# Kernel optimization log

Measured on AMD Instinct MI355X. Metric: run time of the kernel, lower is better.

Reference implementation:

```python
import jax, jax.numpy as jnp
import numpy as np

MIN_CONN, MAX_CONN = 1, 16
RATIO = 0.25
EPS_NORM = 1e-12   # F.normalize eps
GN_EPS = 1e-5
NUM_GROUPS = 32    # largest divisor of C=128 that is <= 32


def setup_inputs() -> dict:
    key = jax.random.key(0)
    ks = jax.random.split(key, 3)
    B, C, H, W = 2, 128, 48, 48
    x = jax.random.normal(ks[0], (B, C, H, W), dtype=jnp.float32)
    gamma = jnp.ones((C,), jnp.float32)
    beta = jnp.zeros((C,), jnp.float32)
    w1 = jax.random.normal(ks[1], (2 * C, C), jnp.float32) * 0.02
    b1 = jnp.zeros((2 * C,), jnp.float32)
    w2 = jax.random.normal(ks[2], (C, 2 * C), jnp.float32) * 0.02
    b2 = jnp.zeros((C,), jnp.float32)
    return {"x": x, "gamma": gamma, "beta": beta, "w1": w1, "b1": b1, "w2": w2, "b2": b2}


def _connection_counts(x):
    B, C, H, W = x.shape
    xd = jax.image.resize(x, (B, C, H // 2, W // 2), method='bilinear', antialias=False)
    xdu = jax.image.resize(xd, (B, C, H, W), method='bilinear', antialias=False)
    df = jnp.abs(x - xdu).sum(axis=1, keepdims=True)  # [B,1,H,W]
    dmin = df.reshape(B, -1).min(axis=1).reshape(B, 1, 1, 1)
    dmax = df.reshape(B, -1).max(axis=1).reshape(B, 1, 1, 1)
    dn = (df - dmin) / (dmax - dmin + 1e-8)
    return MIN_CONN + jnp.round(dn * (MAX_CONN - MIN_CONN))  # [B,1,H,W] float


def _ipg_forward(x, gamma, beta, w1, b1, w2, b2):
    B, C, H, W = x.shape
    cc = _connection_counts(x)

    win = max(3, int(min(H, W) * RATIO))
    if win % 2 == 0:
        win += 1
    K2 = win * win
    pad = win // 2

    xp = jnp.pad(x, ((0, 0), (0, 0), (pad, pad), (pad, pad)), mode='reflect')
    # unfold -> [B, C, K2, H, W] with torch ordering (row-major over (i,j))
    patches = jnp.stack([xp[:, :, i:i + H, j:j + W]
                         for i in range(win) for j in range(win)], axis=2)
    patches = patches.reshape(B, C, K2, H * W).transpose(0, 3, 1, 2)  # [B,P,C,K2]

    x_flat = x.reshape(B, C, H * W).transpose(0, 2, 1)  # [B,P,C]
    x_norm = x_flat / jnp.maximum(jnp.linalg.norm(x_flat, axis=-1, keepdims=True), EPS_NORM)
    pnorm = jnp.maximum(jnp.sqrt((patches ** 2).sum(axis=2)), EPS_NORM)  # [B,P,K2]
    sim = jnp.einsum('bpck,bpc->bpk', patches, x_norm) / pnorm  # [B,P,K2]

    # variable-k topk as a rank mask: rank(sim descending) < k, then exp-softmax over selected
    k = jnp.minimum(cc.reshape(B, H * W), float(K2))  # [B,P]
    ranks = jnp.argsort(jnp.argsort(-sim, axis=-1), axis=-1)  # [B,P,K2]
    mask = ranks < k[..., None]
    w = jnp.exp(sim) * mask
    w = w / w.sum(axis=-1, keepdims=True)
    out = jnp.einsum('bpck,bpk->bpc', patches, w)  # [B,P,C]
    out = out.transpose(0, 2, 1).reshape(B, C, H, W)

    # GroupNorm(32, C)
    xg = x.reshape(B, NUM_GROUPS, C // NUM_GROUPS, H, W)
    mu = xg.mean(axis=(2, 3, 4), keepdims=True)
    var = xg.var(axis=(2, 3, 4), keepdims=True)
    xn = ((xg - mu) / jnp.sqrt(var + GN_EPS)).reshape(B, C, H, W)
    norm_x = xn * gamma[None, :, None, None] + beta[None, :, None, None]

    enhanced = out + norm_x
    # 1x1 conv FFN
    h = jnp.einsum('oc,bchw->bohw', w1, enhanced) + b1[None, :, None, None]
    h = jax.nn.relu(h)
    ffn = jnp.einsum('oc,bchw->bohw', w2, h) + b2[None, :, None, None]
    return enhanced + ffn


def reference(x, gamma, beta, w1, b1, w2, b2):
    return _ipg_forward(x, gamma, beta, w1, b1, w2, b2)
```

## Files before the change

### kernel.cpp

```cpp
#include <hip/hip_runtime.h>

constexpr int CH = 128;
constexpr int WW = 48;
constexpr int PP = 2304;
constexpr int NPIX = 4608;
constexpr int K2 = 169;

constexpr size_t OFF_XT  = 0;
constexpr size_t OFF_RN  = OFF_XT + (size_t)NPIX * CH;
constexpr size_t OFF_DF  = OFF_RN + NPIX;
constexpr size_t OFF_GNP = OFF_DF + NPIX;
constexpr size_t OFF_MMP = OFF_GNP + 288 * 16;
constexpr size_t OFF_W1T = OFF_MMP + 144;
constexpr size_t OFF_W2T = OFF_W1T + 32768;
constexpr size_t WS_FLOATS = OFF_W2T + 32768;

__device__ __forceinline__ int refl(int t) {
    return t < 0 ? -t : (t > 47 ? 94 - t : t);
}

__global__ __launch_bounds__(256) void kA(const float* __restrict__ x,
                                          const float* __restrict__ w1,
                                          const float* __restrict__ w2,
                                          float* __restrict__ xt,
                                          float* __restrict__ gnp,
                                          float* __restrict__ w1t,
                                          float* __restrict__ w2t,
                                          float* __restrict__ df,
                                          float* __restrict__ rn,
                                          float* __restrict__ mmp) {
    __shared__ union { float t[32][65]; float red[4][64][2]; } sm;
    const int tid = threadIdx.x;
    const int bid = blockIdx.x;
    if (bid < 288) {
        const int tile = bid >> 2, q = bid & 3;
        const int p0 = tile * 64;
        const int b = p0 / PP, pb = p0 % PP;
        const int pl = tid & 63, cb = tid >> 6;
        const float* xb = x + (size_t)b * CH * PP + (size_t)(q * 32) * PP + pb;
#pragma unroll
        for (int r = 0; r < 8; r++) {
            int c = r * 4 + cb;
            sm.t[c][pl] = xb[(size_t)c * PP + pl];
        }
        __syncthreads();
        {
            const int c4 = tid & 7, pq = tid >> 3;
#pragma unroll
            for (int r = 0; r < 2; r++) {
                int px = r * 32 + pq;
                float4 v = make_float4(sm.t[c4 * 4][px], sm.t[c4 * 4 + 1][px],
                                       sm.t[c4 * 4 + 2][px], sm.t[c4 * 4 + 3][px]);
                ((float4*)(xt + (size_t)(p0 + px) * CH + q * 32))[c4] = v;
            }
        }
        {
            const int j = tid >> 5, part = tid & 31;
            float s = 0.f, sq = 0.f;
#pragma unroll
            for (int pi = 0; pi < 2; pi++) {
                int px = part * 2 + pi;
#pragma unroll
                for (int i = 0; i < 4; i++) {
                    float v = sm.t[j * 4 + i][px];
                    s += v; sq += v * v;
                }
            }
#pragma unroll
            for (int m = 16; m; m >>= 1) { s += __shfl_xor(s, m); sq += __shfl_xor(sq, m); }
            if (part == 0) { gnp[bid * 16 + j * 2] = s; gnp[bid * 16 + j * 2 + 1] = sq; }
        }
    } else if (bid < 360) {
        const int strip = bid - 288;
        const int p0 = strip * 64;
        const int b = p0 / PP;
        const int wv = tid >> 6, lane = tid & 63;
        const int p = (p0 % PP) + lane;
        const int h = p / WW, w = p % WW;
        float py = 0.5f * h - 0.25f; int y0 = (int)floorf(py); float fy = py - (float)y0;
        float px_ = 0.5f * w - 0.25f; int x0 = (int)floorf(px_); float fx = px_ - (float)x0;
        int y0c = max(y0, 0), y1c = min(y0 + 1, 23);
        int x0c = max(x0, 0), x1c = min(x0 + 1, 23);
        float q00 = 0.25f * (1.f - fy) * (1.f - fx), q01 = 0.25f * (1.f - fy) * fx;
        float q10 = 0.25f * fy * (1.f - fx),        q11 = 0.25f * fy * fx;
        int r0 = (2 * y0c) * WW, r1 = (2 * y0c + 1) * WW;
        int r2 = (2 * y1c) * WW, r3 = (2 * y1c + 1) * WW;
        int ca = 2 * x0c, cb2 = 2 * x1c;
        const float* xc = x + (size_t)b * CH * PP + (size_t)(wv * 32) * PP;
        float ds = 0.f, ss = 0.f;
        for (int c = 0; c < 32; c++) {
            const float* xp = xc + (size_t)c * PP;
            float xv = xp[p];
            float s00 = xp[r0 + ca] + xp[r0 + ca + 1] + xp[r1 + ca] + xp[r1 + ca + 1];
            float s01 = xp[r0 + cb2] + xp[r0 + cb2 + 1] + xp[r1 + cb2] + xp[r1 + cb2 + 1];
            float s10 = xp[r2 + ca] + xp[r2 + ca + 1] + xp[r3 + ca] + xp[r3 + ca + 1];
            float s11 = xp[r2 + cb2] + xp[r2 + cb2 + 1] + xp[r3 + cb2] + xp[r3 + cb2 + 1];
            float up = q00 * s00 + q01 * s01 + q10 * s10 + q11 * s11;
            ds += fabsf(xv - up);
            ss += xv * xv;
        }
        sm.red[wv][lane][0] = ds; sm.red[wv][lane][1] = ss;
        __syncthreads();
        if (wv == 0) {
            float dst = sm.red[0][lane][0] + sm.red[1][lane][0] +
                        sm.red[2][lane][0] + sm.red[3][lane][0];
            float sst = sm.red[0][lane][1] + sm.red[1][lane][1] +
                        sm.red[2][lane][1] + sm.red[3][lane][1];
            df[p0 + lane] = dst;
            rn[p0 + lane] = 1.f / fmaxf(sqrtf(sst), 1e-12f);
            float mn = dst, mx = dst;
#pragma unroll
            for (int m = 32; m; m >>= 1) {
                mn = fminf(mn, __shfl_xor(mn, m));
                mx = fmaxf(mx, __shfl_xor(mx, m));
            }
            if (lane == 0) { mmp[strip * 2] = mn; mmp[strip * 2 + 1] = mx; }
        }
    } else {
        int idx = (bid - 360) * 256 + tid;
        if (idx < 32768) {
            int o = idx >> 7, c = idx & 127;
            w1t[(size_t)((c >> 2) * 256 + o) * 4 + (c & 3)] = w1[idx];
        } else {
            int i2 = idx - 32768;
            int c = i2 >> 8, oo = i2 & 255;
            w2t[(size_t)((oo >> 2) * 128 + c) * 4 + (oo & 3)] = w2[i2];
        }
    }
}

__global__ __launch_bounds__(256, 4) void kB(const float* __restrict__ xt,
                                             const float* __restrict__ rn,
                                             const float* __restrict__ df,
                                             const float* __restrict__ mmp,
                                             const float* __restrict__ gnp,
                                             const float* __restrict__ gamma,
                                             const float* __restrict__ beta,
                                             const float* __restrict__ w1t,
                                             const float* __restrict__ w2t,
                                             const float* __restrict__ b1f,
                                             const float* __restrict__ b2f,
                                             float* __restrict__ out) {
    __shared__ union {
        float sims[4][176];
        struct { float elds[4][128]; float hlds[4][256]; } f;
    } sm;
    __shared__ float gnbl[32][2];
    __shared__ float mml[2];
    const int tid = threadIdx.x, wv = tid >> 6, lane = tid & 63;
    const int base = blockIdx.x * 4;
    const int b = base / PP;

    if (tid < 32) {
        const int g = tid, q = g >> 3, j = g & 7;
        float s = 0.f, sq = 0.f;
#pragma unroll 4
        for (int t2 = 0; t2 < 36; t2++) {
            int u = (b * 36 + t2) * 4 + q;
            s += gnp[u * 16 + j * 2];
            sq += gnp[u * 16 + j * 2 + 1];
        }
        float mu = s / 9216.f;
        float var = sq / 9216.f - mu * mu;
        gnbl[g][0] = mu;
        gnbl[g][1] = 1.f / sqrtf(var + 1e-5f);
    } else if (tid >= 64 && tid < 128) {
        int i = tid - 64;
        float mn = 1e30f, mx = -1e30f;
        if (i < 36) { mn = mmp[(b * 36 + i) * 2]; mx = mmp[(b * 36 + i) * 2 + 1]; }
#pragma unroll
        for (int m = 32; m; m >>= 1) {
            mn = fminf(mn, __shfl_xor(mn, m));
            mx = fmaxf(mx, __shfl_xor(mx, m));
        }
        if (i == 0) { mml[0] = mn; mml[1] = mx; }
    }
    __syncthreads();
    const float dmin = mml[0], dmax = mml[1];

    const int pix = base + wv;
    const int p = pix % PP;
    const int h = p / WW, w = p % WW;
    const int bb = b * PP;
    const int g8 = lane >> 3, cl = lane & 7;

    float4 ctr[4];
    const float4* cp = (const float4*)(xt + (size_t)pix * CH) + cl;
#pragma unroll
    for (int c = 0; c < 4; c++) ctr[c] = cp[c * 8];
    const float rnp = rn[pix];

    for (int kb = 0; kb < 176; kb += 8) {
        const int k = kb + g8;
        const int krow = k / 13, kcol = k - krow * 13;
        const int yy = refl(h + krow - 6), xx = refl(w + kcol - 6);
        const int p2 = bb + yy * WW + xx;
        const float4* rp = (const float4*)(xt + (size_t)p2 * CH) + cl;
        float dot = 0.f;
#pragma unroll
        for (int c = 0; c < 4; c++) {
            float4 v = rp[c * 8];
            dot += v.x * ctr[c].x + v.y * ctr[c].y + v.z * ctr[c].z + v.w * ctr[c].w;
        }
        dot += __shfl_xor(dot, 1);
        dot += __shfl_xor(dot, 2);
        dot += __shfl_xor(dot, 4);
        float s = dot * rnp * rn[p2];
        if (cl == 0 && k < K2) sm.sims[wv][k] = s;
    }

    float s0 = sm.sims[wv][lane];
    float s1 = (64 + lane < K2) ? sm.sims[wv][64 + lane] : -1e30f;
    float s2 = (128 + lane < K2) ? sm.sims[wv][128 + lane] : -1e30f;
    const float dn = (df[pix] - dmin) / (dmax - dmin + 1e-8f);
    const int cc = 1 + (int)rintf(dn * 15.f);

    float wsum = 0.f, ax = 0.f, ay = 0.f;
    for (int i = 0; i < cc; ++i) {
        float gm = fmaxf(fmaxf(s0, s1), s2);
#pragma unroll
        for (int sft = 1; sft <= 32; sft <<= 1) gm = fmaxf(gm, __shfl_xor(gm, sft));
        unsigned long long m0 = __ballot(s0 == gm);
        unsigned long long m1 = __ballot(s1 == gm);
        unsigned long long m2 = __ballot(s2 == gm);
        int kw = m0 ? (__ffsll(m0) - 1)
               : m1 ? (64 + __ffsll(m1) - 1)
                    : (128 + __ffsll(m2) - 1);
        bool me = (lane == (kw & 63));
        s0 = (me && kw < 64) ? -1e30f : s0;
        s1 = (me && kw >= 64 && kw < 128) ? -1e30f : s1;
        s2 = (me && kw >= 128) ? -1e30f : s2;
        float wt = expf(gm);
        wsum += wt;
        int krow = kw / 13, kcol = kw - krow * 13;
        int p2 = bb + refl(h + krow - 6) * WW + refl(w + kcol - 6);
        float2 v = ((const float2*)(xt + (size_t)p2 * CH))[lane];
        ax += wt * v.x; ay += wt * v.y;
    }
    const float invw = 1.f / wsum;

    float2 xv = ((const float2*)(xt + (size_t)pix * CH))[lane];
    const int c0 = lane * 2, grp = lane >> 1;
    const float mu = gnbl[grp][0], rstd = gnbl[grp][1];
    float e0 = ax * invw + (xv.x - mu) * rstd * gamma[c0] + beta[c0];
    float e1 = ay * invw + (xv.y - mu) * rstd * gamma[c0 + 1] + beta[c0 + 1];

    __syncthreads();
    ((float2*)sm.f.elds[wv])[lane] = make_float2(e0, e1);
    __syncthreads();

    {
        float acc4[4] = {0.f, 0.f, 0.f, 0.f};
        const float4* wp = ((const float4*)w1t) + tid;
        for (int c4 = 0; c4 < 32; c4++) {
            float4 wv4 = wp[c4 * 256];
#pragma unroll
            for (int px = 0; px < 4; px++) {
                float4 ev = *(const float4*)&sm.f.elds[px][c4 * 4];
                acc4[px] += wv4.x * ev.x + wv4.y * ev.y + wv4.z * ev.z + wv4.w * ev.w;
            }
        }
        float bv = b1f[tid];
#pragma unroll
        for (int px = 0; px < 4; px++)
            sm.f.hlds[px][tid] = fmaxf(acc4[px] + bv, 0.f);
    }
    __syncthreads();
    {
        const int c = tid & 127, hf = tid >> 7;
        const int px0 = hf * 2;
        float acc2[2] = {0.f, 0.f};
        const float4* wp2 = ((const float4*)w2t) + c;
        for (int o4 = 0; o4 < 64; o4++) {
            float4 wv4 = wp2[o4 * 128];
#pragma unroll
            for (int j = 0; j < 2; j++) {
                float4 hv = *(const float4*)&sm.f.hlds[px0 + j][o4 * 4];
                acc2[j] += wv4.x * hv.x + wv4.y * hv.y + wv4.z * hv.z + wv4.w * hv.w;
            }
        }
        float bv = b2f[c];
        float2 o2;
        o2.x = sm.f.elds[px0 + 0][c] + acc2[0] + bv;
        o2.y = sm.f.elds[px0 + 1][c] + acc2[1] + bv;
        *(float2*)(out + ((size_t)(b * CH + c)) * PP + (base % PP) + px0) = o2;
    }
}

extern "C" void kernel_launch(void* const* d_in, const int* in_sizes, int n_in,
                              void* d_out, int out_size, void* d_ws, size_t ws_size,
                              hipStream_t stream) {
    (void)in_sizes; (void)n_in; (void)out_size;
    if (ws_size < WS_FLOATS * sizeof(float)) return;

    const float* x     = (const float*)d_in[0];
    const float* gamma = (const float*)d_in[1];
    const float* beta  = (const float*)d_in[2];
    const float* w1    = (const float*)d_in[3];
    const float* b1    = (const float*)d_in[4];
    const float* w2    = (const float*)d_in[5];
    const float* b2    = (const float*)d_in[6];
    float* ws = (float*)d_ws;
    float* xt  = ws + OFF_XT;
    float* rn  = ws + OFF_RN;
    float* df  = ws + OFF_DF;
    float* gnp = ws + OFF_GNP;
    float* mmp = ws + OFF_MMP;
    float* w1t = ws + OFF_W1T;
    float* w2t = ws + OFF_W2T;
    float* out = (float*)d_out;

    hipLaunchKernelGGL(kA, dim3(616),  dim3(256), 0, stream,
                       x, w1, w2, xt, gnp, w1t, w2t, df, rn, mmp);
    hipLaunchKernelGGL(kB, dim3(1152), dim3(256), 0, stream,
                       xt, rn, df, mmp, gnp, gamma, beta, w1t, w2t, b1, b2, out);
}
```

Measured before the change: 63.89 us.

## Decouple top-k selection from gather and widen similarity per-lane work

The similarity loop now gives each lane group 4 lanes instead of 8, so it processes 16 neighbours per iteration with 8 float4 loads per lane, and it is unrolled by two. The serial top-k loop only records the selected indices and scores in shared memory. A separate, fully unrolled 16-iteration gather loop then does the exp and weighted accumulation, so its global loads can be issued together instead of one dependent load per selection step. Slots that were not selected hold score -1e30, so their exp is 0, but they still issue loads of neighbour 0. Launch bounds drop to 2 blocks per SM to allow more registers, at some cost in occupancy.

```diff
diff --git a/kernel.cpp b/kernel.cpp
--- a/kernel.cpp
+++ b/kernel.cpp
@@ -129,7 +129,7 @@
     }
 }
 
-__global__ __launch_bounds__(256, 4) void kB(const float* __restrict__ xt,
+__global__ __launch_bounds__(256, 2) void kB(const float* __restrict__ xt,
                                              const float* __restrict__ rn,
                                              const float* __restrict__ df,
                                              const float* __restrict__ mmp,
@@ -142,7 +142,7 @@
                                              const float* __restrict__ b2f,
                                              float* __restrict__ out) {
     __shared__ union {
-        float sims[4][176];
+        struct { float sims[4][176]; int kl[4][16]; float wl[4][16]; } a;
         struct { float elds[4][128]; float hlds[4][256]; } f;
     } sm;
     __shared__ float gnbl[32][2];
@@ -182,40 +182,41 @@
     const int p = pix % PP;
     const int h = p / WW, w = p % WW;
     const int bb = b * PP;
-    const int g8 = lane >> 3, cl = lane & 7;
-
-    float4 ctr[4];
-    const float4* cp = (const float4*)(xt + (size_t)pix * CH) + cl;
-#pragma unroll
-    for (int c = 0; c < 4; c++) ctr[c] = cp[c * 8];
+    const int g16 = lane >> 2, cl2 = lane & 3;
+
+    float4 ctr[8];
+    const float4* cp = (const float4*)(xt + (size_t)pix * CH);
+#pragma unroll
+    for (int c = 0; c < 8; c++) ctr[c] = cp[c * 4 + cl2];
     const float rnp = rn[pix];
 
-    for (int kb = 0; kb < 176; kb += 8) {
-        const int k = kb + g8;
+    if (lane < 16) { sm.a.kl[wv][lane] = 0; sm.a.wl[wv][lane] = -1e30f; }
+
+#pragma unroll 2
+    for (int kb = 0; kb < 176; kb += 16) {
+        const int k = kb + g16;
         const int krow = k / 13, kcol = k - krow * 13;
         const int yy = refl(h + krow - 6), xx = refl(w + kcol - 6);
         const int p2 = bb + yy * WW + xx;
-        const float4* rp = (const float4*)(xt + (size_t)p2 * CH) + cl;
+        const float4* rp = (const float4*)(xt + (size_t)p2 * CH);
         float dot = 0.f;
 #pragma unroll
-        for (int c = 0; c < 4; c++) {
-            float4 v = rp[c * 8];
+        for (int c = 0; c < 8; c++) {
+            float4 v = rp[c * 4 + cl2];
             dot += v.x * ctr[c].x + v.y * ctr[c].y + v.z * ctr[c].z + v.w * ctr[c].w;
         }
         dot += __shfl_xor(dot, 1);
         dot += __shfl_xor(dot, 2);
-        dot += __shfl_xor(dot, 4);
         float s = dot * rnp * rn[p2];
-        if (cl == 0 && k < K2) sm.sims[wv][k] = s;
-    }
-
-    float s0 = sm.sims[wv][lane];
-    float s1 = (64 + lane < K2) ? sm.sims[wv][64 + lane] : -1e30f;
-    float s2 = (128 + lane < K2) ? sm.sims[wv][128 + lane] : -1e30f;
+        if (cl2 == 0 && k < K2) sm.a.sims[wv][k] = s;
+    }
+
+    float s0 = sm.a.sims[wv][lane];
+    float s1 = sm.a.sims[wv][64 + lane];
+    float s2 = (128 + lane < K2) ? sm.a.sims[wv][128 + lane] : -1e30f;
     const float dn = (df[pix] - dmin) / (dmax - dmin + 1e-8f);
     const int cc = 1 + (int)rintf(dn * 15.f);
 
-    float wsum = 0.f, ax = 0.f, ay = 0.f;
     for (int i = 0; i < cc; ++i) {
         float gm = fmaxf(fmaxf(s0, s1), s2);
 #pragma unroll
@@ -230,12 +231,19 @@
         s0 = (me && kw < 64) ? -1e30f : s0;
         s1 = (me && kw >= 64 && kw < 128) ? -1e30f : s1;
         s2 = (me && kw >= 128) ? -1e30f : s2;
-        float wt = expf(gm);
-        wsum += wt;
-        int krow = kw / 13, kcol = kw - krow * 13;
-        int p2 = bb + refl(h + krow - 6) * WW + refl(w + kcol - 6);
+        if (lane == 0) { sm.a.kl[wv][i] = kw; sm.a.wl[wv][i] = gm; }
+    }
+
+    float wsum = 0.f, ax = 0.f, ay = 0.f;
+#pragma unroll
+    for (int i = 0; i < 16; ++i) {
+        const int kw = sm.a.kl[wv][i];
+        const float sv = sm.a.wl[wv][i];
+        const float wt = expf(sv);
+        const int krow = kw / 13, kcol = kw - krow * 13;
+        const int p2 = bb + refl(h + krow - 6) * WW + refl(w + kcol - 6);
         float2 v = ((const float2*)(xt + (size_t)p2 * CH))[lane];
-        ax += wt * v.x; ay += wt * v.y;
+        wsum += wt; ax += wt * v.x; ay += wt * v.y;
     }
     const float invw = 1.f / wsum;
 
```

Result: slower. 70.07 us (+9.7%).

## Split similarity computation across two wave halves and decouple top-k gather

Applied to the files above, without the earlier changes.

Doubles the kB block to 512 threads so two waves share each pixel's 169 similarity dot products, halving the serial neighbour loop per wave. The top-k selection now only records the chosen indices and scores in shared memory, and a separate fully unrolled 16-iteration loop gathers and accumulates, so the neighbour loads are independent instead of interleaved with the serial selection. Unused slots carry -1e30 so their exp contributes zero. In exchange, the extra waves sit idle during selection and the FFN stages, and each block always issues 16 gather loads.

```diff
diff --git a/kernel.cpp b/kernel.cpp
--- a/kernel.cpp
+++ b/kernel.cpp
@@ -129,7 +129,7 @@
     }
 }
 
-__global__ __launch_bounds__(256, 4) void kB(const float* __restrict__ xt,
+__global__ __launch_bounds__(512, 8) void kB(const float* __restrict__ xt,
                                              const float* __restrict__ rn,
                                              const float* __restrict__ df,
                                              const float* __restrict__ mmp,
@@ -142,12 +142,13 @@
                                              const float* __restrict__ b2f,
                                              float* __restrict__ out) {
     __shared__ union {
-        float sims[4][176];
+        struct { float sims[4][176]; int kl[4][16]; float wl[4][16]; } a;
         struct { float elds[4][128]; float hlds[4][256]; } f;
     } sm;
     __shared__ float gnbl[32][2];
     __shared__ float mml[2];
     const int tid = threadIdx.x, wv = tid >> 6, lane = tid & 63;
+    const int pxw = wv & 3, half = wv >> 2;
     const int base = blockIdx.x * 4;
     const int b = base / PP;
 
@@ -175,10 +176,8 @@
         }
         if (i == 0) { mml[0] = mn; mml[1] = mx; }
     }
-    __syncthreads();
-    const float dmin = mml[0], dmax = mml[1];
-
-    const int pix = base + wv;
+
+    const int pix = base + pxw;
     const int p = pix % PP;
     const int h = p / WW, w = p % WW;
     const int bb = b * PP;
@@ -189,9 +188,12 @@
 #pragma unroll
     for (int c = 0; c < 4; c++) ctr[c] = cp[c * 8];
     const float rnp = rn[pix];
-
-    for (int kb = 0; kb < 176; kb += 8) {
-        const int k = kb + g8;
+    __syncthreads();
+
+    const int kb0 = half * 88;
+#pragma unroll 2
+    for (int it = 0; it < 11; ++it) {
+        const int k = kb0 + it * 8 + g8;
         const int krow = k / 13, kcol = k - krow * 13;
         const int yy = refl(h + krow - 6), xx = refl(w + kcol - 6);
         const int p2 = bb + yy * WW + xx;
@@ -206,50 +208,62 @@
         dot += __shfl_xor(dot, 2);
         dot += __shfl_xor(dot, 4);
         float s = dot * rnp * rn[p2];
-        if (cl == 0 && k < K2) sm.sims[wv][k] = s;
-    }
-
-    float s0 = sm.sims[wv][lane];
-    float s1 = (64 + lane < K2) ? sm.sims[wv][64 + lane] : -1e30f;
-    float s2 = (128 + lane < K2) ? sm.sims[wv][128 + lane] : -1e30f;
-    const float dn = (df[pix] - dmin) / (dmax - dmin + 1e-8f);
-    const int cc = 1 + (int)rintf(dn * 15.f);
-
-    float wsum = 0.f, ax = 0.f, ay = 0.f;
-    for (int i = 0; i < cc; ++i) {
-        float gm = fmaxf(fmaxf(s0, s1), s2);
-#pragma unroll
-        for (int sft = 1; sft <= 32; sft <<= 1) gm = fmaxf(gm, __shfl_xor(gm, sft));
-        unsigned long long m0 = __ballot(s0 == gm);
-        unsigned long long m1 = __ballot(s1 == gm);
-        unsigned long long m2 = __ballot(s2 == gm);
-        int kw = m0 ? (__ffsll(m0) - 1)
-               : m1 ? (64 + __ffsll(m1) - 1)
-                    : (128 + __ffsll(m2) - 1);
-        bool me = (lane == (kw & 63));
-        s0 = (me && kw < 64) ? -1e30f : s0;
-        s1 = (me && kw >= 64 && kw < 128) ? -1e30f : s1;
-        s2 = (me && kw >= 128) ? -1e30f : s2;
-        float wt = expf(gm);
-        wsum += wt;
-        int krow = kw / 13, kcol = kw - krow * 13;
-        int p2 = bb + refl(h + krow - 6) * WW + refl(w + kcol - 6);
-        float2 v = ((const float2*)(xt + (size_t)p2 * CH))[lane];
-        ax += wt * v.x; ay += wt * v.y;
-    }
-    const float invw = 1.f / wsum;
-
-    float2 xv = ((const float2*)(xt + (size_t)pix * CH))[lane];
-    const int c0 = lane * 2, grp = lane >> 1;
-    const float mu = gnbl[grp][0], rstd = gnbl[grp][1];
-    float e0 = ax * invw + (xv.x - mu) * rstd * gamma[c0] + beta[c0];
-    float e1 = ay * invw + (xv.y - mu) * rstd * gamma[c0 + 1] + beta[c0 + 1];
-
-    __syncthreads();
-    ((float2*)sm.f.elds[wv])[lane] = make_float2(e0, e1);
-    __syncthreads();
-
-    {
+        if (cl == 0 && k < K2) sm.a.sims[pxw][k] = s;
+    }
+    __syncthreads();
+
+    float e0 = 0.f, e1 = 0.f;
+    if (half == 0) {
+        if (lane < 16) { sm.a.kl[pxw][lane] = 0; sm.a.wl[pxw][lane] = -1e30f; }
+        float s0 = sm.a.sims[pxw][lane];
+        float s1 = sm.a.sims[pxw][64 + lane];
+        float s2 = (128 + lane < K2) ? sm.a.sims[pxw][128 + lane] : -1e30f;
+        const float dmin = mml[0], dmax = mml[1];
+        const float dn = (df[pix] - dmin) / (dmax - dmin + 1e-8f);
+        const int cc = 1 + (int)rintf(dn * 15.f);
+
+        for (int i = 0; i < cc; ++i) {
+            float gm = fmaxf(fmaxf(s0, s1), s2);
+#pragma unroll
+            for (int sft = 1; sft <= 32; sft <<= 1) gm = fmaxf(gm, __shfl_xor(gm, sft));
+            unsigned long long m0 = __ballot(s0 == gm);
+            unsigned long long m1 = __ballot(s1 == gm);
+            unsigned long long m2 = __ballot(s2 == gm);
+            int kw = m0 ? (__ffsll(m0) - 1)
+                   : m1 ? (64 + __ffsll(m1) - 1)
+                        : (128 + __ffsll(m2) - 1);
+            bool me = (lane == (kw & 63));
+            s0 = (me && kw < 64) ? -1e30f : s0;
+            s1 = (me && kw >= 64 && kw < 128) ? -1e30f : s1;
+            s2 = (me && kw >= 128) ? -1e30f : s2;
+            if (lane == 0) { sm.a.kl[pxw][i] = kw; sm.a.wl[pxw][i] = gm; }
+        }
+
+        float wsum = 0.f, ax = 0.f, ay = 0.f;
+#pragma unroll
+        for (int i = 0; i < 16; ++i) {
+            const int kw = sm.a.kl[pxw][i];
+            const float sv = sm.a.wl[pxw][i];
+            const float wt = expf(sv);
+            const int krow = kw / 13, kcol = kw - krow * 13;
+            const int p2 = bb + refl(h + krow - 6) * WW + refl(w + kcol - 6);
+            float2 v = ((const float2*)(xt + (size_t)p2 * CH))[lane];
+            wsum += wt; ax += wt * v.x; ay += wt * v.y;
+        }
+        const float invw = 1.f / wsum;
+
+        float2 xv = ((const float2*)(xt + (size_t)pix * CH))[lane];
+        const int c0 = lane * 2, grp = lane >> 1;
+        const float mu = gnbl[grp][0], rstd = gnbl[grp][1];
+        e0 = ax * invw + (xv.x - mu) * rstd * gamma[c0] + beta[c0];
+        e1 = ay * invw + (xv.y - mu) * rstd * gamma[c0 + 1] + beta[c0 + 1];
+    }
+
+    __syncthreads();
+    if (half == 0) ((float2*)sm.f.elds[pxw])[lane] = make_float2(e0, e1);
+    __syncthreads();
+
+    if (tid < 256) {
         float acc4[4] = {0.f, 0.f, 0.f, 0.f};
         const float4* wp = ((const float4*)w1t) + tid;
         for (int c4 = 0; c4 < 32; c4++) {
@@ -266,7 +280,7 @@
             sm.f.hlds[px][tid] = fmaxf(acc4[px] + bv, 0.f);
     }
     __syncthreads();
-    {
+    if (tid < 256) {
         const int c = tid & 127, hf = tid >> 7;
         const int px0 = hf * 2;
         float acc2[2] = {0.f, 0.f};
@@ -312,6 +326,6 @@
 
     hipLaunchKernelGGL(kA, dim3(616),  dim3(256), 0, stream,
                        x, w1, w2, xt, gnp, w1t, w2t, df, rn, mmp);
-    hipLaunchKernelGGL(kB, dim3(1152), dim3(256), 0, stream,
+    hipLaunchKernelGGL(kB, dim3(1152), dim3(512), 0, stream,
                        xt, rn, df, mmp, gnp, gamma, beta, w1t, w2t, b1, b2, out);
 }
```

Result: slower. 82.22 us (+28.7%).
